# Performance work log

Hardware: AMD Instinct MI355X
Metric: run time of the kernel (lower is better)

## Reference

```python
import jax, jax.numpy as jnp
import numpy as np

B, S, D = 2, 2048, 1024
H = 16
HD = D // H  # 64


def _rope_tables(seq_len, head_dim, dtype=jnp.float32):
    inv_freq = 1.0 / (10000.0 ** (jnp.arange(0, head_dim, 2, dtype=jnp.float32) / head_dim))
    t = jnp.arange(seq_len, dtype=jnp.float32)
    freqs = jnp.einsum('i,j->ij', t, inv_freq)            # [S, HD/2]
    emb = jnp.concatenate([freqs, freqs], axis=-1)        # [S, HD]
    return jnp.cos(emb).astype(dtype)[None, None], jnp.sin(emb).astype(dtype)[None, None]


def _rotate_half(x):
    x1, x2 = x[..., : x.shape[-1] // 2], x[..., x.shape[-1] // 2 :]
    return jnp.concatenate([-x2, x1], axis=-1)


def setup_inputs() -> dict:
    key = jax.random.key(0)
    ks = jax.random.split(key, 9)
    s = 0.02
    return {
        'hidden_states': jax.random.normal(ks[0], (B, S, D), jnp.float32),
        'attention_mask': jnp.zeros((B, 1, S, S), jnp.float32),
        'Wq': jax.random.normal(ks[1], (D, D), jnp.float32) * s,
        'bq': jnp.zeros((D,), jnp.float32),
        'Wk': jax.random.normal(ks[2], (D, D), jnp.float32) * s,
        'bk': jnp.zeros((D,), jnp.float32),
        'Wv': jax.random.normal(ks[3], (D, D), jnp.float32) * s,
        'bv': jnp.zeros((D,), jnp.float32),
        'Wo': jax.random.normal(ks[4], (D, D), jnp.float32) * s,
        'bo': jnp.zeros((D,), jnp.float32),
    }


def reference(hidden_states, attention_mask, Wq, bq, Wk, bk, Wv, bv, Wo, bo):
    b, s = hidden_states.shape[:2]
    q = hidden_states @ Wq.T + bq
    k = hidden_states @ Wk.T + bk
    v = hidden_states @ Wv.T + bv
    # [B, H, S, HD]
    q = q.reshape(b, s, H, HD).transpose(0, 2, 1, 3)
    k = k.reshape(b, s, H, HD).transpose(0, 2, 1, 3)
    v = v.reshape(b, s, H, HD).transpose(0, 2, 1, 3)
    cos, sin = _rope_tables(s, HD, q.dtype)
    q = q * cos + _rotate_half(q) * sin
    k = k * cos + _rotate_half(k) * sin
    scaling = HD ** (-0.5)
    scores = jnp.einsum('bhqd,bhkd->bhqk', q, k) * scaling
    scores = scores / jnp.log(jnp.asarray(float(s), scores.dtype))  # dynamic NTK
    scores = scores + attention_mask
    probs = jax.nn.softmax(scores, axis=-1)
    out = jnp.einsum('bhqk,bhkd->bhqd', probs, v)
    out = out.transpose(0, 2, 1, 3).reshape(b, s, H * HD)
    return out @ Wo.T + bo
```

## Files before the change

### kernel.cpp

```cpp
#include <hip/hip_runtime.h>
#include <math.h>

#define S_LEN 2048
#define NHEAD 16
#define HDIM  64

typedef __attribute__((ext_vector_type(8))) short bf16x8;
typedef __attribute__((ext_vector_type(4))) float f32x4;

__device__ __forceinline__ unsigned short f2bf(float f) {
    union { float f; unsigned u; } v; v.f = f;
    unsigned r = v.u + 0x7fffu + ((v.u >> 16) & 1u);
    return (unsigned short)(r >> 16);
}

__device__ __forceinline__ void gl2lds16(const void* g, void* l) {
    __builtin_amdgcn_global_load_lds(
        (__attribute__((address_space(1))) void*)(void*)(g),
        (__attribute__((address_space(3))) void*)(l), 16, 0, 0);
}

__global__ __launch_bounds__(256) void convert_kernel(
    const float* __restrict__ hs, const float* __restrict__ Wq,
    const float* __restrict__ Wk, const float* __restrict__ Wv,
    const float* __restrict__ Wo, unsigned short* __restrict__ dst,
    float2* __restrict__ rtab)
{
    const int bid = blockIdx.x;
    if (bid >= 8192) {
        const int gid = (bid - 8192) * 256 + threadIdx.x;
        const int s = gid >> 5, i = gid & 31;
        const float l2c = 0.41524101186092029f;
        const float freq = exp2f(-(float)i * l2c);
        const float ang = (float)s * freq;
        float2 cs;
        cs.x = cosf(ang);
        cs.y = sinf(ang);
        rtab[gid] = cs;
        return;
    }
    const int gid = bid * 256 + threadIdx.x;
    const int n = gid << 2;
    const float* src; int off;
    if (n < (4 << 20))      { src = hs; off = n; }
    else if (n < (5 << 20)) { src = Wq; off = n - (4 << 20); }
    else if (n < (6 << 20)) { src = Wk; off = n - (5 << 20); }
    else if (n < (7 << 20)) { src = Wv; off = n - (6 << 20); }
    else                    { src = Wo; off = n - (7 << 20); }
    const float4 v = *(const float4*)(src + off);
    ushort4 o;
    o.x = f2bf(v.x); o.y = f2bf(v.y); o.z = f2bf(v.z); o.w = f2bf(v.w);
    *(ushort4*)(dst + n) = o;
}

__global__ __launch_bounds__(256, 3) void qkv_gemm_kernel(
    const unsigned short* __restrict__ X,
    const unsigned short* __restrict__ Wall,
    const float* __restrict__ bq, const float* __restrict__ bk,
    const float* __restrict__ bv, const float2* __restrict__ rtab,
    unsigned short* __restrict__ qo, unsigned short* __restrict__ ko,
    unsigned short* __restrict__ vo)
{
    __shared__ unsigned short As[128 * 64];
    __shared__ unsigned short Bs[128 * 64];

    const int mat = blockIdx.x >> 3;
    const int n0  = (blockIdx.x & 7) << 7;
    const int m0  = blockIdx.y << 7;
    const unsigned short* W = Wall + (mat << 20);
    const float* bias = (mat == 0) ? bq : (mat == 1) ? bk : bv;
    unsigned short* out = (mat == 0) ? qo : (mat == 1) ? ko : vo;

    const int tid = threadIdx.x;
    const int wave = tid >> 6, lane = tid & 63;
    const int quad = lane >> 4, ln = lane & 15;
    const int wm = (wave >> 1) << 6, wn = (wave & 1) << 6;

    f32x4 acc[4][4] = {};

    for (int k0 = 0; k0 < 1024; k0 += 64) {
        #pragma unroll
        for (int L = 0; L < 4; ++L) {
            const int i = tid + (L << 8);
            const int r = i >> 3, cl = i & 7;
            const int cg = (cl ^ (r & 7)) << 3;
            gl2lds16(X + (m0 + r) * 1024 + k0 + cg, &As[i << 3]);
            gl2lds16(W + (n0 + r) * 1024 + k0 + cg, &Bs[i << 3]);
        }
        __syncthreads();
        #pragma unroll
        for (int s = 0; s < 2; ++s) {
            bf16x8 a[4], b[4];
            #pragma unroll
            for (int t = 0; t < 4; ++t) {
                const int ra = wm + (t << 4) + ln;
                a[t] = *(const bf16x8*)&As[(ra << 6) + ((((s << 2) | quad) ^ (ra & 7)) << 3)];
                const int rb = wn + (t << 4) + ln;
                b[t] = *(const bf16x8*)&Bs[(rb << 6) + ((((s << 2) | quad) ^ (rb & 7)) << 3)];
            }
            #pragma unroll
            for (int i = 0; i < 4; ++i)
                #pragma unroll
                for (int j = 0; j < 4; ++j)
                    acc[i][j] = __builtin_amdgcn_mfma_f32_16x16x32_bf16(a[i], b[j], acc[i][j], 0, 0, 0);
        }
        __syncthreads();
    }

    float bv4[4];
    #pragma unroll
    for (int jt = 0; jt < 4; ++jt) bv4[jt] = bias[n0 + wn + (jt << 4) + ln];

    const int h = (n0 + wn) >> 6;

    #pragma unroll
    for (int i = 0; i < 4; ++i) {
        #pragma unroll
        for (int reg = 0; reg < 4; ++reg) {
            const int m = m0 + wm + (i << 4) + (quad << 2) + reg;
            const int b_ = m >> 11, s_ = m & 2047;
            unsigned short* o = out + ((((b_ << 4) + h) << 11) + s_) * 64;
            if (mat < 2) {
                #pragma unroll
                for (int jl = 0; jl < 2; ++jl) {
                    const int hd = (jl << 4) + ln;
                    const float2 cs = rtab[(s_ << 5) + hd];
                    const float x1 = acc[i][jl][reg] + bv4[jl];
                    const float x2 = acc[i][jl + 2][reg] + bv4[jl + 2];
                    o[hd]      = f2bf(x1 * cs.x - x2 * cs.y);
                    o[hd + 32] = f2bf(x2 * cs.x + x1 * cs.y);
                }
            } else {
                #pragma unroll
                for (int jt = 0; jt < 4; ++jt) {
                    const int hd = (jt << 4) + ln;
                    o[hd] = f2bf(acc[i][jt][reg] + bv4[jt]);
                }
            }
        }
    }
}

__global__ __launch_bounds__(256) void vtrans_kernel(
    const unsigned short* __restrict__ v, unsigned short* __restrict__ vt)
{
    __shared__ unsigned short T[64][66];
    const int bh = blockIdx.x >> 5;
    const int s0 = (blockIdx.x & 31) << 6;
    const int tid = threadIdx.x;
    #pragma unroll
    for (int L = 0; L < 4; ++L) {
        const int i = tid + (L << 8);
        const int r = i >> 4, c4 = (i & 15) << 2;
        const ushort4 in = *(const ushort4*)(v + ((bh << 11) + s0 + r) * 64 + c4);
        T[r][c4 + 0] = in.x; T[r][c4 + 1] = in.y;
        T[r][c4 + 2] = in.z; T[r][c4 + 3] = in.w;
    }
    __syncthreads();
    #pragma unroll
    for (int L = 0; L < 4; ++L) {
        const int i = tid + (L << 8);
        const int hd = i >> 4, c4 = (i & 15) << 2;
        ushort4 o;
        o.x = T[c4 + 0][hd]; o.y = T[c4 + 1][hd];
        o.z = T[c4 + 2][hd]; o.w = T[c4 + 3][hd];
        *(ushort4*)(vt + ((bh << 6) + hd) * 2048 + s0 + c4) = o;
    }
}

__global__ __launch_bounds__(256, 4) void flash_kernel(
    const unsigned short* __restrict__ qb, const unsigned short* __restrict__ kb,
    const unsigned short* __restrict__ vtb, const float* __restrict__ mask,
    unsigned short* __restrict__ attn)
{
    __shared__ unsigned short Ks[2][64 * 64];
    __shared__ unsigned short Vt[2][64 * 64];
    __shared__ unsigned short Ps[64 * 64];

    const int qt = blockIdx.x & 31;
    const int bh = blockIdx.x >> 5;
    const int b_ = bh >> 4, h = bh & 15;
    const int q0 = qt << 6;

    const int tid = threadIdx.x;
    const int wave = tid >> 6, lane = tid & 63;
    const int quad = lane >> 4, ln = lane & 15;

    const unsigned short* qrow = qb + ((size_t)((bh << 11) + q0 + (wave << 4) + ln) << 6);
    bf16x8 qa[2];
    qa[0] = *(const bf16x8*)(qrow + (quad << 3));
    qa[1] = *(const bf16x8*)(qrow + 32 + (quad << 3));

    const float scale = 0.125f / logf(2048.0f);

    const float* mbase = mask + ((size_t)b_ << 22)
                       + ((size_t)(q0 + (wave << 4) + (quad << 2)) << 11) + (ln << 2);

    unsigned short* Pw = Ps + (wave << 10);

    const int i0 = tid, i1 = tid + 256;
    const int r0 = i0 >> 3, c0 = ((i0 & 7) ^ (r0 & 7)) << 3;
    const int r1 = i1 >> 3, c1 = ((i1 & 7) ^ (r1 & 7)) << 3;
    const int p0 = ((r0 & 15) << 2) + (r0 >> 4);
    const int p1 = ((r1 & 15) << 2) + (r1 >> 4);
    const unsigned short* kg0 = kb + ((bh << 11) + p0) * 64 + c0;
    const unsigned short* kg1 = kb + ((bh << 11) + p1) * 64 + c1;
    const unsigned short* vg0 = vtb + ((bh << 6) + r0) * 2048 + c0;
    const unsigned short* vg1 = vtb + ((bh << 6) + r1) * 2048 + c1;

    float l_i[4] = {0.f, 0.f, 0.f, 0.f};
    f32x4 O[4] = {};

    gl2lds16(kg0, &Ks[0][i0 << 3]);
    gl2lds16(kg1, &Ks[0][i1 << 3]);
    gl2lds16(vg0, &Vt[0][i0 << 3]);
    gl2lds16(vg1, &Vt[0][i1 << 3]);
    float4 mcur[4];
    #pragma unroll
    for (int reg = 0; reg < 4; ++reg)
        mcur[reg] = *(const float4*)(mbase + (reg << 11));

    for (int kt = 0; kt < 32; ++kt) {
        const int cur = kt & 1;

        __syncthreads();

        float4 mnext[4];
        if (kt < 31) {
            const int kn = (kt + 1) << 6;
            gl2lds16(kg0 + (kn << 6), &Ks[cur ^ 1][i0 << 3]);
            gl2lds16(kg1 + (kn << 6), &Ks[cur ^ 1][i1 << 3]);
            gl2lds16(vg0 + kn, &Vt[cur ^ 1][i0 << 3]);
            gl2lds16(vg1 + kn, &Vt[cur ^ 1][i1 << 3]);
            #pragma unroll
            for (int reg = 0; reg < 4; ++reg)
                mnext[reg] = *(const float4*)(mbase + kn + (reg << 11));
        }

        f32x4 sacc[4] = {};
        #pragma unroll
        for (int s = 0; s < 2; ++s) {
            bf16x8 bfr[4];
            #pragma unroll
            for (int j = 0; j < 4; ++j) {
                const int r = (j << 4) + ln;
                bfr[j] = *(const bf16x8*)&Ks[cur][(r << 6) + ((((s << 2) | quad) ^ (r & 7)) << 3)];
            }
            #pragma unroll
            for (int j = 0; j < 4; ++j)
                sacc[j] = __builtin_amdgcn_mfma_f32_16x16x32_bf16(qa[s], bfr[j], sacc[j], 0, 0, 0);
        }

        #pragma unroll
        for (int reg = 0; reg < 4; ++reg) {
            const int pr = (quad << 2) + reg;
            const float m0f = mcur[reg].x, m1f = mcur[reg].y,
                        m2f = mcur[reg].z, m3f = mcur[reg].w;
            float p[4];
            p[0] = __expf(fmaf(sacc[0][reg], scale, m0f));
            p[1] = __expf(fmaf(sacc[1][reg], scale, m1f));
            p[2] = __expf(fmaf(sacc[2][reg], scale, m2f));
            p[3] = __expf(fmaf(sacc[3][reg], scale, m3f));
            l_i[reg] += (p[0] + p[1]) + (p[2] + p[3]);
            unsigned u0 = __float_as_uint(p[0]) + 0x8000u;
            unsigned u1 = __float_as_uint(p[1]) + 0x8000u;
            unsigned u2 = __float_as_uint(p[2]) + 0x8000u;
            unsigned u3 = __float_as_uint(p[3]) + 0x8000u;
            uint2 w;
            w.x = __builtin_amdgcn_perm(u1, u0, 0x07060302u);
            w.y = __builtin_amdgcn_perm(u3, u2, 0x07060302u);
            const int e = (pr << 6) + ((((ln >> 1) ^ (pr & 7)) << 3)) + ((ln & 1) << 2);
            *(uint2*)&Pw[e] = w;
        }

        #pragma unroll
        for (int s = 0; s < 2; ++s) {
            const bf16x8 a = *(const bf16x8*)&Pw[(ln << 6) + ((((s << 2) | quad) ^ (ln & 7)) << 3)];
            bf16x8 bfr[4];
            #pragma unroll
            for (int j = 0; j < 4; ++j) {
                const int r = (j << 4) + ln;
                bfr[j] = *(const bf16x8*)&Vt[cur][(r << 6) + ((((s << 2) | quad) ^ (r & 7)) << 3)];
            }
            #pragma unroll
            for (int j = 0; j < 4; ++j)
                O[j] = __builtin_amdgcn_mfma_f32_16x16x32_bf16(a, bfr[j], O[j], 0, 0, 0);
        }

        if (kt < 31) {
            #pragma unroll
            for (int reg = 0; reg < 4; ++reg)
                mcur[reg] = mnext[reg];
        }
    }

    #pragma unroll
    for (int reg = 0; reg < 4; ++reg) {
        float l = l_i[reg];
        l += __shfl_xor(l, 1);
        l += __shfl_xor(l, 2);
        l += __shfl_xor(l, 4);
        l += __shfl_xor(l, 8);
        const float inv = 1.0f / l;
        const int qr = q0 + (wave << 4) + (quad << 2) + reg;
        unsigned short* op = attn + (((size_t)((b_ << 11) + qr)) << 10) + (h << 6);
        #pragma unroll
        for (int j = 0; j < 4; ++j)
            op[(j << 4) + ln] = f2bf(O[j][reg] * inv);
    }
}

__global__ __launch_bounds__(256, 3) void out_gemm_kernel(
    const unsigned short* __restrict__ X, const unsigned short* __restrict__ W,
    const float* __restrict__ bias, float* __restrict__ out)
{
    __shared__ unsigned short As[128 * 64];
    __shared__ unsigned short Bs[128 * 64];

    const int n0 = blockIdx.x << 7;
    const int m0 = blockIdx.y << 7;
    const int tid = threadIdx.x;
    const int wave = tid >> 6, lane = tid & 63;
    const int quad = lane >> 4, ln = lane & 15;
    const int wm = (wave >> 1) << 6, wn = (wave & 1) << 6;

    f32x4 acc[4][4] = {};

    for (int k0 = 0; k0 < 1024; k0 += 64) {
        #pragma unroll
        for (int L = 0; L < 4; ++L) {
            const int i = tid + (L << 8);
            const int r = i >> 3, cl = i & 7;
            const int cg = (cl ^ (r & 7)) << 3;
            gl2lds16(X + (m0 + r) * 1024 + k0 + cg, &As[i << 3]);
            gl2lds16(W + (n0 + r) * 1024 + k0 + cg, &Bs[i << 3]);
        }
        __syncthreads();
        #pragma unroll
        for (int s = 0; s < 2; ++s) {
            bf16x8 a[4], b[4];
            #pragma unroll
            for (int t = 0; t < 4; ++t) {
                const int ra = wm + (t << 4) + ln;
                a[t] = *(const bf16x8*)&As[(ra << 6) + ((((s << 2) | quad) ^ (ra & 7)) << 3)];
                const int rb = wn + (t << 4) + ln;
                b[t] = *(const bf16x8*)&Bs[(rb << 6) + ((((s << 2) | quad) ^ (rb & 7)) << 3)];
            }
            #pragma unroll
            for (int i = 0; i < 4; ++i)
                #pragma unroll
                for (int j = 0; j < 4; ++j)
                    acc[i][j] = __builtin_amdgcn_mfma_f32_16x16x32_bf16(a[i], b[j], acc[i][j], 0, 0, 0);
        }
        __syncthreads();
    }

    float bv4[4];
    #pragma unroll
    for (int jt = 0; jt < 4; ++jt) bv4[jt] = bias[n0 + wn + (jt << 4) + ln];

    #pragma unroll
    for (int i = 0; i < 4; ++i)
        #pragma unroll
        for (int reg = 0; reg < 4; ++reg) {
            const int m = m0 + wm + (i << 4) + (quad << 2) + reg;
            #pragma unroll
            for (int jt = 0; jt < 4; ++jt) {
                const int n = n0 + wn + (jt << 4) + ln;
                out[m * 1024 + n] = acc[i][jt][reg] + bv4[jt];
            }
        }
}

extern "C" void kernel_launch(void* const* d_in, const int* in_sizes, int n_in,
                              void* d_out, int out_size, void* d_ws, size_t ws_size,
                              hipStream_t stream)
{
    const float* hs   = (const float*)d_in[0];
    const float* mask = (const float*)d_in[1];
    const float* Wq   = (const float*)d_in[2];
    const float* bq   = (const float*)d_in[3];
    const float* Wk   = (const float*)d_in[4];
    const float* bk   = (const float*)d_in[5];
    const float* Wv   = (const float*)d_in[6];
    const float* bv   = (const float*)d_in[7];
    const float* Wo   = (const float*)d_in[8];
    const float* bo   = (const float*)d_in[9];

    unsigned short* ws = (unsigned short*)d_ws;
    const size_t M1 = (size_t)1 << 20;
    unsigned short* hsb   = ws;
    unsigned short* wall  = ws + 4 * M1;
    unsigned short* wob   = ws + 7 * M1;
    unsigned short* qbf   = ws + 8 * M1;
    unsigned short* kbf   = ws + 12 * M1;
    unsigned short* vbf   = ws + 16 * M1;
    unsigned short* vtb   = ws + 20 * M1;
    unsigned short* attnb = ws + 24 * M1;
    float2*         rtab  = (float2*)(ws + 28 * M1);

    convert_kernel<<<8448, 256, 0, stream>>>(hs, Wq, Wk, Wv, Wo, ws, rtab);
    qkv_gemm_kernel<<<dim3(24, 32), 256, 0, stream>>>(hsb, wall, bq, bk, bv, rtab, qbf, kbf, vbf);
    vtrans_kernel<<<1024, 256, 0, stream>>>(vbf, vtb);
    flash_kernel<<<1024, 256, 0, stream>>>(qbf, kbf, vtb, mask, attnb);
    out_gemm_kernel<<<dim3(8, 32), 256, 0, stream>>>(attnb, wob, bo, (float*)d_out);
}
```

Before: 237.9 us.

## Permute weight rows in GEMM tiles so epilogues write vectorized contiguous outputs

```diff
diff --git a/kernel.cpp b/kernel.cpp
--- a/kernel.cpp
+++ b/kernel.cpp
@@ -76,16 +76,29 @@
     const int quad = lane >> 4, ln = lane & 15;
     const int wm = (wave >> 1) << 6, wn = (wave & 1) << 6;
 
+    const unsigned short* xptr[4];
+    const unsigned short* wptr[4];
+    #pragma unroll
+    for (int L = 0; L < 4; ++L) {
+        const int i = tid + (L << 8);
+        const int r = i >> 3, cl = i & 7;
+        const int cg = (cl ^ (r & 7)) << 3;
+        const int rq = r & 63;
+        const int tau = (mat < 2)
+            ? ((r & 64) | ((rq & 15) << 1) | ((rq >> 4) & 1) | (((rq >> 5) & 1) << 5))
+            : ((r & 64) | ((rq & 15) << 2) | (rq >> 4));
+        xptr[L] = X + (m0 + r) * 1024 + cg;
+        wptr[L] = W + (n0 + tau) * 1024 + cg;
+    }
+
     f32x4 acc[4][4] = {};
 
     for (int k0 = 0; k0 < 1024; k0 += 64) {
         #pragma unroll
         for (int L = 0; L < 4; ++L) {
             const int i = tid + (L << 8);
-            const int r = i >> 3, cl = i & 7;
-            const int cg = (cl ^ (r & 7)) << 3;
-            gl2lds16(X + (m0 + r) * 1024 + k0 + cg, &As[i << 3]);
-            gl2lds16(W + (n0 + r) * 1024 + k0 + cg, &Bs[i << 3]);
+            gl2lds16(xptr[L] + k0, &As[i << 3]);
+            gl2lds16(wptr[L] + k0, &Bs[i << 3]);
         }
         __syncthreads();
         #pragma unroll
@@ -107,37 +120,52 @@
         __syncthreads();
     }
 
-    float bv4[4];
-    #pragma unroll
-    for (int jt = 0; jt < 4; ++jt) bv4[jt] = bias[n0 + wn + (jt << 4) + ln];
-
     const int h = (n0 + wn) >> 6;
 
-    #pragma unroll
-    for (int i = 0; i < 4; ++i) {
-        #pragma unroll
-        for (int reg = 0; reg < 4; ++reg) {
-            const int m = m0 + wm + (i << 4) + (quad << 2) + reg;
-            const int b_ = m >> 11, s_ = m & 2047;
-            unsigned short* o = out + ((((b_ << 4) + h) << 11) + s_) * 64;
-            if (mat < 2) {
-                #pragma unroll
-                for (int jl = 0; jl < 2; ++jl) {
-                    const int hd = (jl << 4) + ln;
-                    const float2 cs = rtab[(s_ << 5) + hd];
-                    const float x1 = acc[i][jl][reg] + bv4[jl];
-                    const float x2 = acc[i][jl + 2][reg] + bv4[jl + 2];
-                    o[hd]      = f2bf(x1 * cs.x - x2 * cs.y);
-                    o[hd + 32] = f2bf(x2 * cs.x + x1 * cs.y);
-                }
-            } else {
-                #pragma unroll
-                for (int jt = 0; jt < 4; ++jt) {
-                    const int hd = (jt << 4) + ln;
-                    o[hd] = f2bf(acc[i][jt][reg] + bv4[jt]);
-                }
-            }
-        }
+    if (mat < 2) {
+        const int nb = n0 + wn + (ln << 1);
+        const float b0 = bias[nb],      b1 = bias[nb + 1];
+        const float b2 = bias[nb + 32], b3 = bias[nb + 33];
+        #pragma unroll
+        for (int i = 0; i < 4; ++i) {
+            #pragma unroll
+            for (int reg = 0; reg < 4; ++reg) {
+                const int m = m0 + wm + (i << 4) + (quad << 2) + reg;
+                const int b_ = m >> 11, s_ = m & 2047;
+                unsigned short* o = out + ((((b_ << 4) + h) << 11) + s_) * 64;
+                const float4 cs = *(const float4*)(rtab + (s_ << 5) + (ln << 1));
+                const float x1a = acc[i][0][reg] + b0, x1b = acc[i][1][reg] + b1;
+                const float x2a = acc[i][2][reg] + b2, x2b = acc[i][3][reg] + b3;
+                const float r0a = x1a * cs.x - x2a * cs.y;
+                const float r0b = x1b * cs.z - x2b * cs.w;
+                const float r1a = x2a * cs.x + x1a * cs.y;
+                const float r1b = x2b * cs.z + x1b * cs.w;
+                const unsigned ua = __float_as_uint(r0a) + 0x8000u;
+                const unsigned ub = __float_as_uint(r0b) + 0x8000u;
+                const unsigned uc = __float_as_uint(r1a) + 0x8000u;
+                const unsigned ud = __float_as_uint(r1b) + 0x8000u;
+                *(unsigned*)(o + (ln << 1))      = __builtin_amdgcn_perm(ub, ua, 0x07060302u);
+                *(unsigned*)(o + 32 + (ln << 1)) = __builtin_amdgcn_perm(ud, uc, 0x07060302u);
+            }
+        }
+    } else {
+        const float4 bv4 = *(const float4*)(bias + n0 + wn + (ln << 2));
+        #pragma unroll
+        for (int i = 0; i < 4; ++i)
+            #pragma unroll
+            for (int reg = 0; reg < 4; ++reg) {
+                const int m = m0 + wm + (i << 4) + (quad << 2) + reg;
+                const int b_ = m >> 11, s_ = m & 2047;
+                unsigned short* o = out + ((((b_ << 4) + h) << 11) + s_) * 64;
+                const unsigned ua = __float_as_uint(acc[i][0][reg] + bv4.x) + 0x8000u;
+                const unsigned ub = __float_as_uint(acc[i][1][reg] + bv4.y) + 0x8000u;
+                const unsigned uc = __float_as_uint(acc[i][2][reg] + bv4.z) + 0x8000u;
+                const unsigned ud = __float_as_uint(acc[i][3][reg] + bv4.w) + 0x8000u;
+                uint2 w;
+                w.x = __builtin_amdgcn_perm(ub, ua, 0x07060302u);
+                w.y = __builtin_amdgcn_perm(ud, uc, 0x07060302u);
+                *(uint2*)(o + (ln << 2)) = w;
+            }
     }
 }
 
@@ -324,16 +352,27 @@
     const int quad = lane >> 4, ln = lane & 15;
     const int wm = (wave >> 1) << 6, wn = (wave & 1) << 6;
 
+    const unsigned short* xptr[4];
+    const unsigned short* wptr[4];
+    #pragma unroll
+    for (int L = 0; L < 4; ++L) {
+        const int i = tid + (L << 8);
+        const int r = i >> 3, cl = i & 7;
+        const int cg = (cl ^ (r & 7)) << 3;
+        const int rq = r & 63;
+        const int tau = (r & 64) | ((rq & 15) << 2) | (rq >> 4);
+        xptr[L] = X + (m0 + r) * 1024 + cg;
+        wptr[L] = W + (n0 + tau) * 1024 + cg;
+    }
+
     f32x4 acc[4][4] = {};
 
     for (int k0 = 0; k0 < 1024; k0 += 64) {
         #pragma unroll
         for (int L = 0; L < 4; ++L) {
             const int i = tid + (L << 8);
-            const int r = i >> 3, cl = i & 7;
-            const int cg = (cl ^ (r & 7)) << 3;
-            gl2lds16(X + (m0 + r) * 1024 + k0 + cg, &As[i << 3]);
-            gl2lds16(W + (n0 + r) * 1024 + k0 + cg, &Bs[i << 3]);
+            gl2lds16(xptr[L] + k0, &As[i << 3]);
+            gl2lds16(wptr[L] + k0, &Bs[i << 3]);
         }
         __syncthreads();
         #pragma unroll
@@ -355,20 +394,19 @@
         __syncthreads();
     }
 
-    float bv4[4];
-    #pragma unroll
-    for (int jt = 0; jt < 4; ++jt) bv4[jt] = bias[n0 + wn + (jt << 4) + ln];
+    const float4 bv4 = *(const float4*)(bias + n0 + wn + (ln << 2));
 
     #pragma unroll
     for (int i = 0; i < 4; ++i)
         #pragma unroll
         for (int reg = 0; reg < 4; ++reg) {
             const int m = m0 + wm + (i << 4) + (quad << 2) + reg;
-            #pragma unroll
-            for (int jt = 0; jt < 4; ++jt) {
-                const int n = n0 + wn + (jt << 4) + ln;
-                out[m * 1024 + n] = acc[i][jt][reg] + bv4[jt];
-            }
+            float4 ov;
+            ov.x = acc[i][0][reg] + bv4.x;
+            ov.y = acc[i][1][reg] + bv4.y;
+            ov.z = acc[i][2][reg] + bv4.z;
+            ov.w = acc[i][3][reg] + bv4.w;
+            *(float4*)(out + m * 1024 + n0 + wn + (ln << 2)) = ov;
         }
 }
 
```

Result: faster. 225.2 us (-5.3%).
